# Performance work log

Measured on AMD Instinct MI355X. Metric: run time of the kernel, lower is better.

Reference implementation:

```python
import jax, jax.numpy as jnp
import numpy as np

B, T, C, H = 2, 2048, 2048, 16
D = C // H  # head size = 128
ROPE_BASE = 10000.0


def setup_inputs() -> dict:
    key = jax.random.key(0)
    k1, k2, k3 = jax.random.split(key, 3)
    scale = 1.0 / np.sqrt(C)
    x = jax.random.normal(k1, (B, T, C), dtype=jnp.float32)
    w_qkv = jax.random.normal(k2, (3 * C, C), dtype=jnp.float32) * scale
    w_o = jax.random.normal(k3, (C, C), dtype=jnp.float32) * scale
    # rope cache: complex exp(i * pos * theta_j), stored as cos/sin, shape [T, D//2]
    inv_freq = 1.0 / (ROPE_BASE ** (np.arange(0, D, 2, dtype=np.float32) / D))  # [D//2]
    angles = np.arange(T, dtype=np.float32)[:, None] * inv_freq[None, :]        # [T, D//2]
    rope_cos = jnp.asarray(np.cos(angles))
    rope_sin = jnp.asarray(np.sin(angles))
    return {"x": x, "w_qkv": w_qkv, "w_o": w_o, "rope_cos": rope_cos, "rope_sin": rope_sin}


def _apply_rope(x, cos, sin):
    # x: [B, T, H, D]; cos/sin: [T, D//2]
    xr = x.reshape(*x.shape[:-1], D // 2, 2)
    x0, x1 = xr[..., 0], xr[..., 1]
    c = cos[None, :, None, :]
    s = sin[None, :, None, :]
    # complex multiply (x0 + i x1) * (c + i s)
    out = jnp.stack([x0 * c - x1 * s, x0 * s + x1 * c], axis=-1)
    return out.reshape(x.shape)


def reference(x, w_qkv, w_o, rope_cos, rope_sin):
    Bs, Ts, Cs = x.shape
    qkv = jnp.einsum('btc,ec->bte', x, w_qkv)  # [B, T, 3C]
    q, k, v = jnp.split(qkv, 3, axis=-1)
    q = q.reshape(Bs, Ts, H, D)
    k = k.reshape(Bs, Ts, H, D)
    v = v.reshape(Bs, Ts, H, D)
    q = _apply_rope(q, rope_cos[:Ts], rope_sin[:Ts])
    k = _apply_rope(k, rope_cos[:Ts], rope_sin[:Ts])
    scores = jnp.einsum('bthd,bshd->bhts', q, k) / jnp.sqrt(jnp.float32(D))
    causal = jnp.tril(jnp.ones((Ts, Ts), dtype=bool))
    scores = jnp.where(causal[None, None], scores, jnp.finfo(scores.dtype).min)
    attn = jax.nn.softmax(scores, axis=-1)
    y = jnp.einsum('bhts,bshd->bthd', attn, v).reshape(Bs, Ts, Cs)
    return jnp.einsum('btc,oc->bto', y, w_o)
```

## Files before the change

### kernel.cpp

```cpp
#include <hip/hip_runtime.h>
#include <cstdint>
#include <cstddef>

#define DEVI __device__ __forceinline__

typedef __attribute__((ext_vector_type(8))) short short8;
typedef __attribute__((ext_vector_type(4))) float f32x4;
typedef __attribute__((ext_vector_type(16))) float f32x16;
typedef __attribute__((ext_vector_type(4))) unsigned int u32x4;

static constexpr int Bdim = 2, T = 2048, C = 2048, H = 16, D = 128;
static constexpr int CQ = 3 * C;

DEVI unsigned short f2bf(float f) {
  unsigned int u = __float_as_uint(f);
  u = (u + 0x7fffu + ((u >> 16) & 1u)) >> 16;
  return (unsigned short)u;
}
DEVI float bf2f(unsigned int u) { return __uint_as_float(u << 16); }

DEVI unsigned int cvtpk(float lo, float hi) {
  unsigned int r;
  asm("v_cvt_pk_bf16_f32 %0, %1, %2" : "=v"(r) : "v"(lo), "v"(hi));
  return r;
}

DEVI void gload_lds16(const void* g, void* l) {
  __builtin_amdgcn_global_load_lds((const __attribute__((address_space(1))) void*)g,
                                   (__attribute__((address_space(3))) void*)l, 16, 0, 0);
}

__global__ __launch_bounds__(256) void convert_bf16(const float* __restrict__ src,
                                                    unsigned short* __restrict__ dst, int n) {
  const int i = (blockIdx.x * 256 + threadIdx.x) * 4;
  if (i >= n) return;
  float4 v = *(const float4*)&src[i];
  uint2 o;
  o.x = (unsigned)f2bf(v.x) | ((unsigned)f2bf(v.y) << 16);
  o.y = (unsigned)f2bf(v.z) | ((unsigned)f2bf(v.w) << 16);
  *(uint2*)&dst[i] = o;
}

template <int OUT_BF16>
__global__ __launch_bounds__(256) void gemm_bt(const unsigned short* __restrict__ A,
                                               const unsigned short* __restrict__ Bm,
                                               void* __restrict__ outp,
                                               int M, int N, int Kd) {
  __shared__ __align__(16) unsigned short lds_a[128 * 64];
  __shared__ __align__(16) unsigned short lds_b[128 * 64];
  const int tid = threadIdx.x;
  const int wid = tid >> 6, lane = tid & 63;
  const int lg = lane >> 4, lc = lane & 15;

  const int nwg = gridDim.x * gridDim.y;
  const int bid0 = blockIdx.y * gridDim.x + blockIdx.x;
  const int lid = (bid0 & 7) * (nwg >> 3) + (bid0 >> 3);
  const int m0 = (lid / gridDim.x) * 128;
  const int n0 = (lid % gridDim.x) * 128;

  const int wr = (wid >> 1) * 64, wc = (wid & 1) * 64;
  const int srow = wid * 8 + (lane >> 3);
  const int schunk = lane & 7;

  f32x4 acc[4][4] = {};

  for (int k0 = 0; k0 < Kd; k0 += 64) {
    __syncthreads();
#pragma unroll
    for (int j = 0; j < 4; ++j) {
      const int row = j * 32 + srow;
      const int cc = schunk ^ (row & 7);
      gload_lds16(&A[(size_t)(m0 + row) * Kd + k0 + cc * 8], &lds_a[j * 2048 + wid * 512]);
      gload_lds16(&Bm[(size_t)(n0 + row) * Kd + k0 + cc * 8], &lds_b[j * 2048 + wid * 512]);
    }
    __syncthreads();
    __builtin_amdgcn_s_setprio(1);
#pragma unroll
    for (int kk = 0; kk < 2; ++kk) {
      short8 af[4], bf[4];
#pragma unroll
      for (int m = 0; m < 4; ++m) {
        const int row = wr + m * 16 + lc;
        af[m] = *(const short8*)&lds_a[row * 64 + (((kk * 4 + lg) ^ (row & 7)) * 8)];
      }
#pragma unroll
      for (int n = 0; n < 4; ++n) {
        const int row = wc + n * 16 + lc;
        bf[n] = *(const short8*)&lds_b[row * 64 + (((kk * 4 + lg) ^ (row & 7)) * 8)];
      }
#pragma unroll
      for (int m = 0; m < 4; ++m)
#pragma unroll
        for (int n = 0; n < 4; ++n)
          acc[m][n] = __builtin_amdgcn_mfma_f32_16x16x32_bf16(af[m], bf[n], acc[m][n], 0, 0, 0);
    }
    __builtin_amdgcn_s_setprio(0);
  }

#pragma unroll
  for (int m = 0; m < 4; ++m)
#pragma unroll
    for (int n = 0; n < 4; ++n)
#pragma unroll
      for (int r = 0; r < 4; ++r) {
        const int row = m0 + wr + m * 16 + lg * 4 + r;
        const int col = n0 + wc + n * 16 + lc;
        const float v = acc[m][n][r];
        if (OUT_BF16)
          ((unsigned short*)outp)[(size_t)row * N + col] = f2bf(v);
        else
          ((float*)outp)[(size_t)row * N + col] = v;
      }
}

__global__ __launch_bounds__(256) void rope_vt_kernel(const unsigned short* __restrict__ qkv,
                                                      const float* __restrict__ cosb,
                                                      const float* __restrict__ sinb,
                                                      unsigned short* __restrict__ Qr,
                                                      unsigned short* __restrict__ Kr,
                                                      unsigned short* __restrict__ Vt) {
  if (blockIdx.x < 16384) {
    const int idx = blockIdx.x * 256 + threadIdx.x;
    const int i = idx & 63;
    const int h = (idx >> 6) & (H - 1);
    const int tg = idx >> 10;
    const int t = tg & (T - 1);
    const int b = tg >> 11;
    const float c = cosb[t * 64 + i], s = sinb[t * 64 + i];
    const unsigned short* row = qkv + (size_t)tg * CQ;
    const unsigned int q = *(const unsigned int*)&row[h * D + 2 * i];
    const unsigned int k = *(const unsigned int*)&row[C + h * D + 2 * i];
    const float q0 = bf2f(q & 0xffffu), q1 = bf2f(q >> 16);
    const float k0 = bf2f(k & 0xffffu), k1 = bf2f(k >> 16);
    const float SC = 0.08838834764831845f * 1.4426950408889634f;
    const float q0r = (q0 * c - q1 * s) * SC, q1r = (q0 * s + q1 * c) * SC;
    const float k0r = k0 * c - k1 * s, k1r = k0 * s + k1 * c;
    const size_t off = ((size_t)(b * H + h) * T + t) * D + 2 * i;
    *(unsigned int*)&Qr[off] = (unsigned)f2bf(q0r) | ((unsigned)f2bf(q1r) << 16);
    *(unsigned int*)&Kr[off] = (unsigned)f2bf(k0r) | ((unsigned)f2bf(k1r) << 16);
  } else {
    __shared__ unsigned short tile[64][65];
    const int bid2 = blockIdx.x - 16384;
    const int t0 = (bid2 & 31) * 64;
    const int d0 = ((bid2 >> 5) & 1) * 64;
    const int bh = bid2 >> 6, b = bh >> 4, h = bh & (H - 1);
    const int tx = threadIdx.x & 63, ty = threadIdx.x >> 6;
#pragma unroll
    for (int rr = 0; rr < 64; rr += 4)
      tile[rr + ty][tx] = qkv[(size_t)(b * T + t0 + rr + ty) * CQ + 2 * C + h * D + d0 + tx];
    __syncthreads();
#pragma unroll
    for (int rr = 0; rr < 64; rr += 4)
      Vt[((size_t)bh * D + d0 + rr + ty) * T + t0 + tx] = tile[tx][rr + ty];
  }
}

__global__ __launch_bounds__(256, 2) void flash_attn(const unsigned short* __restrict__ Q,
                                                     const unsigned short* __restrict__ K,
                                                     const unsigned short* __restrict__ Vt,
                                                     unsigned short* __restrict__ Y) {
  __shared__ __align__(16) unsigned short ldsK[64 * 128];
  __shared__ __align__(16) unsigned short ldsV[64 * 128];

  const int bid = blockIdx.x;
  const int lid = (bid & 7) * 64 + (bid >> 3);
  const int bh = lid >> 4;
  const int qt = 15 - (lid & 15);
  const int wid = threadIdx.x >> 6;
  const int lane = threadIdx.x & 63;
  const int l31 = lane & 31, l15 = lane & 15;
  const int hi = lane >> 5;
  const int b = bh >> 4, h = bh & (H - 1);
  const int q0w = qt * 128 + wid * 32;
  const int qrow = q0w + l31;

  const unsigned short* Qh = Q + (size_t)bh * T * D;
  const unsigned short* Kh = K + (size_t)bh * T * D;
  const unsigned short* Vh = Vt + (size_t)bh * D * T;

  const int sr = lane >> 4;

  short8 qf[8];
#pragma unroll
  for (int ds = 0; ds < 8; ++ds)
    qf[ds] = *(const short8*)&Qh[(size_t)qrow * D + ds * 16 + hi * 8];

  f32x16 oacc[4] = {};
  float m_run = -1e30f, l_run = 0.f;

  u32x4 rK[4], rV[4];

#pragma unroll
  for (int j = 0; j < 4; ++j) {
    const int r0 = (wid * 4 + j) * 4;
    const int row = r0 + sr;
    const int cc = l15 ^ (row & 15);
    rK[j] = *(const u32x4*)&Kh[(size_t)row * D + cc * 8];
    const int cv = l15 ^ (row & 15);
    const int d = row + ((cv >> 3) << 6);
    rV[j] = *(const u32x4*)&Vh[(size_t)d * T + (cv & 7) * 8];
  }

  const int ntb = 2 * qt + 2;
  for (int t = 0; t < ntb; ++t) {
    const int kv0 = t * 64;

    __builtin_amdgcn_s_barrier();

#pragma unroll
    for (int j = 0; j < 4; ++j) {
      const int r0 = (wid * 4 + j) * 4;
      *(u32x4*)((char*)ldsK + r0 * 256 + lane * 16) = rK[j];
      *(u32x4*)((char*)ldsV + r0 * 256 + lane * 16) = rV[j];
    }
    asm volatile("s_waitcnt lgkmcnt(0)" ::: "memory");
    __builtin_amdgcn_s_barrier();
    __builtin_amdgcn_sched_barrier(0);

    if (t + 1 < ntb) {
      const int kvn = kv0 + 64;
#pragma unroll
      for (int j = 0; j < 4; ++j) {
        const int r0 = (wid * 4 + j) * 4;
        const int row = r0 + sr;
        const int cc = l15 ^ (row & 15);
        rK[j] = *(const u32x4*)&Kh[(size_t)(kvn + row) * D + cc * 8];
        const int d = row + ((cc >> 3) << 6);
        rV[j] = *(const u32x4*)&Vh[(size_t)d * T + kvn + (cc & 7) * 8];
      }
    }
    __builtin_amdgcn_sched_barrier(0);

    if (kv0 <= q0w + 31) {
      f32x16 s0 = {}, s1 = {};
      __builtin_amdgcn_s_setprio(1);
#pragma unroll
      for (int ds = 0; ds < 8; ++ds) {
        const int cs = ((ds * 2 + hi) ^ l15) * 8;
        const short8 k0 = *(const short8*)&ldsK[l31 * 128 + cs];
        const short8 k1 = *(const short8*)&ldsK[(32 + l31) * 128 + cs];
        s0 = __builtin_amdgcn_mfma_f32_32x32x16_bf16(k0, qf[ds], s0, 0, 0, 0);
        s1 = __builtin_amdgcn_mfma_f32_32x32x16_bf16(k1, qf[ds], s1, 0, 0, 0);
      }
      __builtin_amdgcn_s_setprio(0);

      if (kv0 + 63 > q0w) {
#pragma unroll
        for (int r = 0; r < 16; ++r) {
          const int kvr = kv0 + (r & 3) + 8 * (r >> 2) + 4 * hi;
          s0[r] = (kvr <= qrow) ? s0[r] : -1e30f;
          s1[r] = (kvr + 32 <= qrow) ? s1[r] : -1e30f;
        }
      }

      float mt[8];
#pragma unroll
      for (int r = 0; r < 8; ++r)
        mt[r] = fmaxf(fmaxf(s0[r], s0[r + 8]), fmaxf(s1[r], s1[r + 8]));
#pragma unroll
      for (int r = 0; r < 4; ++r) mt[r] = fmaxf(mt[r], mt[r + 4]);
      float mx = fmaxf(fmaxf(mt[0], mt[1]), fmaxf(mt[2], mt[3]));
      mx = fmaxf(mx, __shfl_xor(mx, 32));
      const float mnew = fmaxf(m_run, mx);
      if (__any(mnew > m_run)) {
        const float f = exp2f(m_run - mnew);
        m_run = mnew;
        l_run *= f;
#pragma unroll
        for (int blk = 0; blk < 4; ++blk) oacc[blk] *= f;
      }
#pragma unroll
      for (int r = 0; r < 16; ++r) {
        s0[r] = exp2f(s0[r] - m_run);
        s1[r] = exp2f(s1[r] - m_run);
      }
      {
        float a0 = 0.f, a1 = 0.f, a2 = 0.f, a3 = 0.f;
#pragma unroll
        for (int r = 0; r < 16; r += 4) {
          a0 += s0[r] + s1[r];
          a1 += s0[r + 1] + s1[r + 1];
          a2 += s0[r + 2] + s1[r + 2];
          a3 += s0[r + 3] + s1[r + 3];
        }
        l_run += (a0 + a1) + (a2 + a3);
      }

      __builtin_amdgcn_s_setprio(1);
#pragma unroll
      for (int ks = 0; ks < 4; ++ks) {
        const int rb = (ks & 1) * 8;
        const f32x16& S = (ks < 2) ? s0 : s1;
        const unsigned int w0 = cvtpk(S[rb + 0], S[rb + 1]);
        const unsigned int w1 = cvtpk(S[rb + 2], S[rb + 3]);
        const unsigned int w2 = cvtpk(S[rb + 4], S[rb + 5]);
        const unsigned int w3 = cvtpk(S[rb + 6], S[rb + 7]);
        const unsigned int x0 = (unsigned int)__shfl_xor((int)w0, 32);
        const unsigned int x1 = (unsigned int)__shfl_xor((int)w1, 32);
        const unsigned int x2 = (unsigned int)__shfl_xor((int)w2, 32);
        const unsigned int x3 = (unsigned int)__shfl_xor((int)w3, 32);
        u32x4 av;
        av[0] = hi ? x2 : w0;
        av[1] = hi ? x3 : w1;
        av[2] = hi ? w2 : x0;
        av[3] = hi ? w3 : x1;
        const short8 pf = __builtin_bit_cast(short8, av);
#pragma unroll
        for (int blk = 0; blk < 4; ++blk) {
          const int row2 = (blk & 1) * 32 + l31;
          const int cs = ((((blk >> 1) * 8) + ks * 2 + hi) ^ l15) * 8;
          const short8 vf = *(const short8*)&ldsV[row2 * 128 + cs];
          oacc[blk] = __builtin_amdgcn_mfma_f32_32x32x16_bf16(vf, pf, oacc[blk], 0, 0, 0);
        }
      }
      __builtin_amdgcn_s_setprio(0);
    }
  }

  const float l = l_run + __shfl_xor(l_run, 32);
  const float inv = 1.0f / l;
  unsigned short* yrow = Y + ((size_t)(b * T + qrow)) * C + h * D;
#pragma unroll
  for (int blk = 0; blk < 4; ++blk)
#pragma unroll
    for (int g = 0; g < 4; ++g) {
      const int d0 = blk * 32 + 8 * g + 4 * hi;
      uint2 st;
      st.x = cvtpk(oacc[blk][4 * g + 0] * inv, oacc[blk][4 * g + 1] * inv);
      st.y = cvtpk(oacc[blk][4 * g + 2] * inv, oacc[blk][4 * g + 3] * inv);
      *(uint2*)&yrow[d0] = st;
    }
}

extern "C" void kernel_launch(void* const* d_in, const int* in_sizes, int n_in,
                              void* d_out, int out_size, void* d_ws, size_t ws_size,
                              hipStream_t stream) {
  const float* x = (const float*)d_in[0];
  const float* wqkv = (const float*)d_in[1];
  const float* wo = (const float*)d_in[2];
  const float* rc = (const float*)d_in[3];
  const float* rs = (const float*)d_in[4];
  float* out = (float*)d_out;
  char* ws = (char*)d_ws;

  unsigned short* xb    = (unsigned short*)(ws + 0);
  unsigned short* wqkvb = (unsigned short*)(ws + 16777216);
  unsigned short* qkv   = (unsigned short*)(ws + 41943040);
  unsigned short* Qr    = (unsigned short*)(ws + 92274688);
  unsigned short* Kr    = (unsigned short*)(ws + 109051904);
  unsigned short* Vt  = xb;
  unsigned short* Yb  = qkv;
  unsigned short* wob = wqkvb;

  convert_bf16<<<8192, 256, 0, stream>>>(x, xb, Bdim * T * C);
  convert_bf16<<<12288, 256, 0, stream>>>(wqkv, wqkvb, CQ * C);
  gemm_bt<1><<<dim3(CQ / 128, (Bdim * T) / 128), 256, 0, stream>>>(xb, wqkvb, (void*)qkv,
                                                                   Bdim * T, CQ, C);
  rope_vt_kernel<<<18432, 256, 0, stream>>>(qkv, rc, rs, Qr, Kr, Vt);
  convert_bf16<<<4096, 256, 0, stream>>>(wo, wob, C * C);
  flash_attn<<<512, 256, 0, stream>>>(Qr, Kr, Vt, Yb);
  gemm_bt<0><<<dim3(C / 128, (Bdim * T) / 128), 256, 0, stream>>>(Yb, wob, (void*)out,
                                                                  Bdim * T, C, C);
}
```

Before: 283.2 us.

## Fuse all fp32-to-bf16 weight/input conversions into one launch; drop GEMM tile swizzle

Merges the three separate bf16 conversion kernels into a single launch that picks its source and destination buffer from the block index. The w_o copy moves into its own workspace region so it can be converted up front instead of between rope and attention. Separately, the GEMM drops its block-index remapping, which grouped tiles to share data in cache, and uses plain row-major tile assignment. Fewer launches save overhead, but losing the swizzle may hurt L2 reuse in the large GEMMs.

```diff
diff --git a/kernel.cpp b/kernel.cpp
--- a/kernel.cpp
+++ b/kernel.cpp
@@ -30,10 +30,23 @@
                                    (__attribute__((address_space(3))) void*)l, 16, 0, 0);
 }
 
-__global__ __launch_bounds__(256) void convert_bf16(const float* __restrict__ src,
-                                                    unsigned short* __restrict__ dst, int n) {
-  const int i = (blockIdx.x * 256 + threadIdx.x) * 4;
-  if (i >= n) return;
+__global__ __launch_bounds__(256) void convert_all(const float* __restrict__ x,
+                                                   const float* __restrict__ wqkv,
+                                                   const float* __restrict__ wo,
+                                                   unsigned short* __restrict__ xb,
+                                                   unsigned short* __restrict__ wqkvb,
+                                                   unsigned short* __restrict__ wob) {
+  int bid = blockIdx.x;
+  const float* src;
+  unsigned short* dst;
+  if (bid < 8192) {
+    src = x; dst = xb;
+  } else if (bid < 8192 + 12288) {
+    bid -= 8192; src = wqkv; dst = wqkvb;
+  } else {
+    bid -= 8192 + 12288; src = wo; dst = wob;
+  }
+  const int i = (bid * 256 + threadIdx.x) * 4;
   float4 v = *(const float4*)&src[i];
   uint2 o;
   o.x = (unsigned)f2bf(v.x) | ((unsigned)f2bf(v.y) << 16);
@@ -51,13 +64,7 @@
   const int tid = threadIdx.x;
   const int wid = tid >> 6, lane = tid & 63;
   const int lg = lane >> 4, lc = lane & 15;
-
-  const int nwg = gridDim.x * gridDim.y;
-  const int bid0 = blockIdx.y * gridDim.x + blockIdx.x;
-  const int lid = (bid0 & 7) * (nwg >> 3) + (bid0 >> 3);
-  const int m0 = (lid / gridDim.x) * 128;
-  const int n0 = (lid % gridDim.x) * 128;
-
+  const int m0 = blockIdx.y * 128, n0 = blockIdx.x * 128;
   const int wr = (wid >> 1) * 64, wc = (wid & 1) * 64;
   const int srow = wid * 8 + (lane >> 3);
   const int schunk = lane & 7;
@@ -348,16 +355,14 @@
   unsigned short* qkv   = (unsigned short*)(ws + 41943040);
   unsigned short* Qr    = (unsigned short*)(ws + 92274688);
   unsigned short* Kr    = (unsigned short*)(ws + 109051904);
+  unsigned short* wob   = (unsigned short*)(ws + 125829120);
   unsigned short* Vt  = xb;
   unsigned short* Yb  = qkv;
-  unsigned short* wob = wqkvb;
-
-  convert_bf16<<<8192, 256, 0, stream>>>(x, xb, Bdim * T * C);
-  convert_bf16<<<12288, 256, 0, stream>>>(wqkv, wqkvb, CQ * C);
+
+  convert_all<<<8192 + 12288 + 4096, 256, 0, stream>>>(x, wqkv, wo, xb, wqkvb, wob);
   gemm_bt<1><<<dim3(CQ / 128, (Bdim * T) / 128), 256, 0, stream>>>(xb, wqkvb, (void*)qkv,
                                                                    Bdim * T, CQ, C);
   rope_vt_kernel<<<18432, 256, 0, stream>>>(qkv, rc, rs, Qr, Kr, Vt);
-  convert_bf16<<<4096, 256, 0, stream>>>(wo, wob, C * C);
   flash_attn<<<512, 256, 0, stream>>>(Qr, Kr, Vt, Yb);
   gemm_bt<0><<<dim3(C / 128, (Bdim * T) / 128), 256, 0, stream>>>(Yb, wob, (void*)out,
                                                                   Bdim * T, C, C);
```

Result: faster. 267.2 us, median of 2 (-5.7%).
